# Kernel optimization log

Measured on AMD Instinct MI355X. Metric: run time of the kernel, lower is better.

## Reference

```python
import jax, jax.numpy as jnp
import numpy as np

D = 256        # d_model
E = 1024       # num_experts (== 4*d_model, required by the broadcast in forward)
F = 4 * D      # expert output width (== E)
N = 4096       # tokens; must be >= E since forward indexes weights[0..E-1]


def setup_inputs() -> dict:
    key = jax.random.key(0)
    k_x, k_gw, k_ew, k_eb = jax.random.split(key, 4)
    x = jax.random.normal(k_x, (N, D), dtype=jnp.float32)
    gate_W = jax.random.normal(k_gw, (D, E), dtype=jnp.float32) * 0.02
    gate_b = jnp.zeros((E,), dtype=jnp.float32)
    expert_W = jax.random.normal(k_ew, (E, D, F), dtype=jnp.float32) * 0.02
    expert_b = jax.random.normal(k_eb, (E, F), dtype=jnp.float32) * 0.02
    return {"x": x, "gate_W": gate_W, "gate_b": gate_b,
            "expert_W": expert_W, "expert_b": expert_b}


def reference(x, gate_W, gate_b, expert_W, expert_b):
    # weights: [N, E] softmax over experts
    weights = jax.nn.softmax(x @ gate_W + gate_b, axis=-1)
    # Original: out = sum_i weights[i] * (x @ W_i + b_i)
    # weights[i] is ROW i (token i) of the gate softmax, shape [E] == [F],
    # broadcast over tokens. Collapse the sum over experts into an effective
    # weight matrix instead of materializing [E, N, F]:
    w = weights[:E]                               # [E, F] rows 0..E-1
    W_eff = jnp.einsum('ef,edf->df', w, expert_W)  # [D, F]
    b_eff = jnp.einsum('ef,ef->f', w, expert_b)    # [F]
    return x @ W_eff + b_eff                       # [N, F]
```

## Files before the change

kernel.cpp:

```cpp
#include <hip/hip_runtime.h>
#include <math.h>


#define DD 256
#define EE 1024
#define FF 1024
#define NN 4096

typedef float f32x4 __attribute__((ext_vector_type(4)));

__global__ __launch_bounds__(256) void gate_kernel(const float* __restrict__ x,
                                                   const float* __restrict__ gW,
                                                   const float* __restrict__ gb,
                                                   float* __restrict__ w_out) {
    __shared__ float xs[4 * DD];
    __shared__ float ls[4 * EE];
    const int tid = threadIdx.x;
    const int r0 = blockIdx.x * 4;

    ((float4*)xs)[tid] = ((const float4*)(x + (size_t)r0 * DD))[tid];
    __syncthreads();

    float4 a0 = {0,0,0,0}, a1 = {0,0,0,0}, a2 = {0,0,0,0}, a3 = {0,0,0,0};
    const float4* gw4 = (const float4*)gW;
    #pragma unroll 4
    for (int d = 0; d < DD; ++d) {
        float4 g = gw4[d * 256 + tid];
        float x0 = xs[0*DD + d], x1 = xs[1*DD + d], x2 = xs[2*DD + d], x3 = xs[3*DD + d];
        a0.x += x0*g.x; a0.y += x0*g.y; a0.z += x0*g.z; a0.w += x0*g.w;
        a1.x += x1*g.x; a1.y += x1*g.y; a1.z += x1*g.z; a1.w += x1*g.w;
        a2.x += x2*g.x; a2.y += x2*g.y; a2.z += x2*g.z; a2.w += x2*g.w;
        a3.x += x3*g.x; a3.y += x3*g.y; a3.z += x3*g.z; a3.w += x3*g.w;
    }
    float4 b = ((const float4*)gb)[tid];
    a0.x += b.x; a0.y += b.y; a0.z += b.z; a0.w += b.w;
    a1.x += b.x; a1.y += b.y; a1.z += b.z; a1.w += b.w;
    a2.x += b.x; a2.y += b.y; a2.z += b.z; a2.w += b.w;
    a3.x += b.x; a3.y += b.y; a3.z += b.z; a3.w += b.w;
    ((float4*)&ls[0*EE])[tid] = a0;
    ((float4*)&ls[1*EE])[tid] = a1;
    ((float4*)&ls[2*EE])[tid] = a2;
    ((float4*)&ls[3*EE])[tid] = a3;
    __syncthreads();

    const int lane = tid & 63;
    const int row = tid >> 6;
    float vals[16];
    float m = -3.0e38f;
    #pragma unroll
    for (int i = 0; i < 16; ++i) {
        vals[i] = ls[row * EE + i * 64 + lane];
        m = fmaxf(m, vals[i]);
    }
    #pragma unroll
    for (int off = 1; off < 64; off <<= 1) m = fmaxf(m, __shfl_xor(m, off));
    float s = 0.0f;
    #pragma unroll
    for (int i = 0; i < 16; ++i) {
        vals[i] = __expf(vals[i] - m);
        s += vals[i];
    }
    #pragma unroll
    for (int off = 1; off < 64; off <<= 1) s += __shfl_xor(s, off);
    const float inv = 1.0f / s;
    float* wrow = w_out + (size_t)(r0 + row) * EE;
    #pragma unroll
    for (int i = 0; i < 16; ++i) wrow[i * 64 + lane] = vals[i] * inv;
}

__global__ __launch_bounds__(256) void weff_kernel(const float* __restrict__ eW,
                                                   const float* __restrict__ eb,
                                                   const float* __restrict__ w,
                                                   float* __restrict__ weff) {
    const int tid = threadIdx.x;
    const int f = tid * 4;
    const int b = blockIdx.x;

    if (b < 16) {
        const int e0 = b * 64;
        const float* pw = w  + (size_t)e0 * EE + f;
        const float* pb = eb + (size_t)e0 * FF + f;
        f32x4 acc = {0.f, 0.f, 0.f, 0.f};
        #pragma unroll 4
        for (int i = 0; i < 64; ++i) {
            f32x4 wv = *(const f32x4*)pw;
            f32x4 a  = __builtin_nontemporal_load((const f32x4*)pb);
            acc += wv * a;
            pw += EE;
            pb += FF;
        }
        float* dst = weff + (size_t)DD * FF + f;
        atomicAdd(dst + 0, acc.x);
        atomicAdd(dst + 1, acc.y);
        atomicAdd(dst + 2, acc.z);
        atomicAdd(dst + 3, acc.w);
        return;
    }

    const int m = b - 16;
    const int dgroup = m >> 4;
    const int echunk = m & 15;
    const int e0 = echunk * 64;
    const int d0 = dgroup * 8;

    const float* pw = w  + (size_t)e0 * EE + f;
    const float* pe = eW + (size_t)e0 * DD * FF + (size_t)d0 * FF + f;

    f32x4 acc[8];
    #pragma unroll
    for (int k = 0; k < 8; ++k) acc[k] = (f32x4){0.f, 0.f, 0.f, 0.f};

    #pragma unroll 2
    for (int i = 0; i < 64; ++i) {
        f32x4 wv = *(const f32x4*)pw;
        f32x4 a[8];
        #pragma unroll
        for (int k = 0; k < 8; ++k)
            a[k] = __builtin_nontemporal_load((const f32x4*)(pe + (size_t)k * FF));
        #pragma unroll
        for (int k = 0; k < 8; ++k)
            acc[k] += wv * a[k];
        pw += EE;
        pe += (size_t)DD * FF;
    }

    #pragma unroll
    for (int k = 0; k < 8; ++k) {
        float* dst = weff + (size_t)(d0 + k) * FF + f;
        atomicAdd(dst + 0, acc[k].x);
        atomicAdd(dst + 1, acc[k].y);
        atomicAdd(dst + 2, acc[k].z);
        atomicAdd(dst + 3, acc[k].w);
    }
}

__global__ __launch_bounds__(256) void out_kernel(const float* __restrict__ x,
                                                  const float* __restrict__ weff,
                                                  float* __restrict__ out) {
    __shared__ float xs[8 * DD];
    const int tid = threadIdx.x;
    const int n0 = blockIdx.x * 8;

    {
        const f32x4* xsrc = (const f32x4*)(x + (size_t)n0 * DD);
        f32x4* xd = (f32x4*)xs;
        #pragma unroll
        for (int k = 0; k < 2; ++k) xd[tid + k * 256] = xsrc[tid + k * 256];
    }
    __syncthreads();

    f32x4 acc[8];
    #pragma unroll
    for (int r = 0; r < 8; ++r) acc[r] = (f32x4){0.f, 0.f, 0.f, 0.f};

    const f32x4* wp = (const f32x4*)weff + tid;
    #pragma unroll 4
    for (int d = 0; d < DD; ++d) {
        f32x4 g = wp[(size_t)d * 256];
        #pragma unroll
        for (int r = 0; r < 8; ++r) {
            float xv = xs[r * DD + d];
            acc[r] += g * xv;
        }
    }

    f32x4 bv = ((const f32x4*)(weff + (size_t)DD * FF))[tid];
    #pragma unroll
    for (int r = 0; r < 8; ++r) {
        f32x4 o = acc[r] + bv;
        __builtin_nontemporal_store(o, (f32x4*)(out + (size_t)(n0 + r) * FF) + tid);
    }
}

extern "C" void kernel_launch(void* const* d_in, const int* in_sizes, int n_in,
                              void* d_out, int out_size, void* d_ws, size_t ws_size,
                              hipStream_t stream) {
    const float* x  = (const float*)d_in[0];
    const float* gW = (const float*)d_in[1];
    const float* gb = (const float*)d_in[2];
    const float* eW = (const float*)d_in[3];
    const float* eb = (const float*)d_in[4];
    float* out = (float*)d_out;

    float* ws   = (float*)d_ws;
    float* w    = ws;
    float* weff = ws + (size_t)EE * EE;

    hipMemsetAsync(weff, 0, (size_t)(DD + 1) * FF * sizeof(float), stream);

    gate_kernel<<<dim3(256), dim3(256), 0, stream>>>(x, gW, gb, w);
    weff_kernel<<<dim3(528), dim3(256), 0, stream>>>(eW, eb, w, weff);
    out_kernel<<<dim3(512), dim3(256), 0, stream>>>(x, weff, out);
}
```

Measured before the change: 1.439 ms.

## Replace atomic W_eff accumulation with partial buffers and a separate reduce kernel

Splits the expert dimension into 32 chunks of 32 instead of 16 of 64, giving twice as many blocks. Each block writes its partial W_eff slice to a private workspace buffer instead of issuing float atomics. A new reduce kernel then sums the 32 partials, which also removes the memset. This avoids atomic contention and improves occupancy on the bandwidth-bound 1 GB expert-weight stream, at the cost of about 34 MB of extra partial traffic and one more launch.

```diff
diff --git a/kernel.cpp b/kernel.cpp
--- a/kernel.cpp
+++ b/kernel.cpp
@@ -68,40 +68,37 @@
     for (int i = 0; i < 16; ++i) wrow[i * 64 + lane] = vals[i] * inv;
 }
 
-__global__ __launch_bounds__(256) void weff_kernel(const float* __restrict__ eW,
-                                                   const float* __restrict__ eb,
-                                                   const float* __restrict__ w,
-                                                   float* __restrict__ weff) {
+__global__ __launch_bounds__(256) void weff_partial_kernel(const float* __restrict__ eW,
+                                                           const float* __restrict__ eb,
+                                                           const float* __restrict__ w,
+                                                           float* __restrict__ part) {
     const int tid = threadIdx.x;
     const int f = tid * 4;
     const int b = blockIdx.x;
 
-    if (b < 16) {
-        const int e0 = b * 64;
+    if (b < 32) {
+        const int ec = b;
+        const int e0 = ec * 32;
         const float* pw = w  + (size_t)e0 * EE + f;
         const float* pb = eb + (size_t)e0 * FF + f;
         f32x4 acc = {0.f, 0.f, 0.f, 0.f};
         #pragma unroll 4
-        for (int i = 0; i < 64; ++i) {
+        for (int i = 0; i < 32; ++i) {
             f32x4 wv = *(const f32x4*)pw;
             f32x4 a  = __builtin_nontemporal_load((const f32x4*)pb);
             acc += wv * a;
             pw += EE;
             pb += FF;
         }
-        float* dst = weff + (size_t)DD * FF + f;
-        atomicAdd(dst + 0, acc.x);
-        atomicAdd(dst + 1, acc.y);
-        atomicAdd(dst + 2, acc.z);
-        atomicAdd(dst + 3, acc.w);
+        *(f32x4*)(part + (size_t)ec * (257 * FF) + (size_t)256 * FF + f) = acc;
         return;
     }
 
-    const int m = b - 16;
-    const int dgroup = m >> 4;
-    const int echunk = m & 15;
-    const int e0 = echunk * 64;
-    const int d0 = dgroup * 8;
+    const int m = b - 32;
+    const int dg = m >> 5;
+    const int ec = m & 31;
+    const int e0 = ec * 32;
+    const int d0 = dg * 8;
 
     const float* pw = w  + (size_t)e0 * EE + f;
     const float* pe = eW + (size_t)e0 * DD * FF + (size_t)d0 * FF + f;
@@ -111,7 +108,7 @@
     for (int k = 0; k < 8; ++k) acc[k] = (f32x4){0.f, 0.f, 0.f, 0.f};
 
     #pragma unroll 2
-    for (int i = 0; i < 64; ++i) {
+    for (int i = 0; i < 32; ++i) {
         f32x4 wv = *(const f32x4*)pw;
         f32x4 a[8];
         #pragma unroll
@@ -124,14 +121,24 @@
         pe += (size_t)DD * FF;
     }
 
-    #pragma unroll
-    for (int k = 0; k < 8; ++k) {
-        float* dst = weff + (size_t)(d0 + k) * FF + f;
-        atomicAdd(dst + 0, acc[k].x);
-        atomicAdd(dst + 1, acc[k].y);
-        atomicAdd(dst + 2, acc[k].z);
-        atomicAdd(dst + 3, acc[k].w);
-    }
+    float* dst = part + (size_t)ec * (257 * FF) + (size_t)d0 * FF + f;
+    #pragma unroll
+    for (int k = 0; k < 8; ++k)
+        *(f32x4*)(dst + (size_t)k * FF) = acc[k];
+}
+
+__global__ __launch_bounds__(256) void weff_reduce_kernel(const float* __restrict__ part,
+                                                          float* __restrict__ weff) {
+    const int tid = threadIdx.x;
+    const int slice = blockIdx.x;
+    const float* p = part + (size_t)slice * FF + (size_t)tid * 4;
+    f32x4 acc = {0.f, 0.f, 0.f, 0.f};
+    #pragma unroll 8
+    for (int ec = 0; ec < 32; ++ec) {
+        acc += __builtin_nontemporal_load((const f32x4*)p);
+        p += (size_t)257 * FF;
+    }
+    *(f32x4*)(weff + (size_t)slice * FF + (size_t)tid * 4) = acc;
 }
 
 __global__ __launch_bounds__(256) void out_kernel(const float* __restrict__ x,
@@ -185,10 +192,10 @@
     float* ws   = (float*)d_ws;
     float* w    = ws;
     float* weff = ws + (size_t)EE * EE;
-
-    hipMemsetAsync(weff, 0, (size_t)(DD + 1) * FF * sizeof(float), stream);
+    float* part = weff + (size_t)(DD + 1) * FF;
 
     gate_kernel<<<dim3(256), dim3(256), 0, stream>>>(x, gW, gb, w);
-    weff_kernel<<<dim3(528), dim3(256), 0, stream>>>(eW, eb, w, weff);
+    weff_partial_kernel<<<dim3(1056), dim3(256), 0, stream>>>(eW, eb, w, part);
+    weff_reduce_kernel<<<dim3(257), dim3(256), 0, stream>>>(part, weff);
     out_kernel<<<dim3(512), dim3(256), 0, stream>>>(x, weff, out);
 }
```

Measured after the change: 1.394 ms. 3.1% less time.
